# Kernel optimization log

Hardware: AMD Instinct MI355X
Metric: run time of the kernel (lower is better)

Reference implementation:

```python
import jax, jax.numpy as jnp
import numpy as np

V = 100000
E = 1600000
IN_CH = 128
HEADS = 4
OUT_CH = 16
NEG_SLOPE = 0.2


def setup_inputs() -> dict:
    key = jax.random.key(0)
    k1, k2, k3, k4, k5 = jax.random.split(key, 5)
    x = jax.random.normal(k1, (V, IN_CH), dtype=jnp.float32)
    edge_index = jax.random.randint(k2, (2, E), 0, V, dtype=jnp.int32)
    # Xavier-ish scaled params
    W = jax.random.normal(k3, (IN_CH, HEADS * OUT_CH), dtype=jnp.float32) / np.sqrt(IN_CH)
    a_src = jax.random.normal(k4, (HEADS, OUT_CH), dtype=jnp.float32) / np.sqrt(OUT_CH)
    a_dst = jax.random.normal(k5, (HEADS, OUT_CH), dtype=jnp.float32) / np.sqrt(OUT_CH)
    return {"x": x, "edge_index": edge_index, "W": W, "a_src": a_src, "a_dst": a_dst}


def reference(x, edge_index, W, a_src, a_dst):
    v = x.shape[0]
    h, cout = a_src.shape
    z = (x @ W).reshape(v, h, cout)                      # [V,H,C]
    src, dst = edge_index[0], edge_index[1]
    # per-node attention logits, then gather at edges (same math as gather-then-dot)
    e_src = jnp.einsum("vhc,hc->vh", z, a_src)           # [V,H]
    e_dst = jnp.einsum("vhc,hc->vh", z, a_dst)           # [V,H]
    e = jax.nn.leaky_relu(e_src[src] + e_dst[dst], NEG_SLOPE)  # [E,H]
    # scatter softmax over dst per head
    m = jax.ops.segment_max(e, dst, num_segments=v)      # [V,H]
    # nodes with no incoming edges get -inf max; edges never reference them
    exp_e = jnp.exp(e - m[dst])                          # [E,H]
    denom = jax.ops.segment_sum(exp_e, dst, num_segments=v)  # [V,H]
    alpha = exp_e / (denom[dst] + 1e-9)                  # [E,H]
    # scatter aggregation of weighted source features
    agg = jax.ops.segment_sum(z[src] * alpha[:, :, None], dst, num_segments=v)  # [V,H,C]
    out = jax.nn.elu(agg)
    return out.reshape(v, h * cout)
```

## Files before the change

### kernel.cpp

```cpp
#include <hip/hip_runtime.h>
#include <hip/hip_bf16.h>
#include <cstdint>

#define NV 100000
#define NE 1600000
#define KIN 128
#define NH 4
#define NC 16
#define NF 64
#define NBKT 782
#define BCAP 2432
#define EPW 16
#define BINWG 391
#define GEMMWG 1563
#define XSTR 136

typedef __attribute__((ext_vector_type(8))) short bf16x8;
typedef __attribute__((ext_vector_type(4))) float f32x4;

__device__ __forceinline__ short f2bf(float f) {
    unsigned u = __float_as_uint(f);
    return (short)((u + 0x7FFFu + ((u >> 16) & 1u)) >> 16);
}

__device__ __forceinline__ unsigned enc11(float w) {
    unsigned t = (__float_as_uint(w) + 0x10000u) >> 17;
    t = min(max(t, 7168u), 9215u);
    return t - 7168u;
}

__global__ __launch_bounds__(256) void k_prep(
    const float* __restrict__ W, short* __restrict__ wfrag,
    int* __restrict__ gcur)
{
    const int t = threadIdx.x;
    for (int i = t; i < NBKT; i += 256) gcur[i] = 0;
#pragma unroll
    for (int it = 0; it < 4; ++it) {
        const int idx = it * 256 + t;
        const int lane = idx & 63;
        const int ctks = idx >> 6;
        const int ct = ctks >> 2, ks = ctks & 3;
        const int n = lane & 15, quad = lane >> 4;
        short* dst = wfrag + (size_t)idx * 8;
#pragma unroll
        for (int j = 0; j < 8; ++j) {
            const int k = ks * 32 + quad * 8 + j;
            dst[j] = f2bf(W[k * NF + ct * 16 + n]);
        }
    }
}

__global__ __launch_bounds__(256) void k_front(
    const float* __restrict__ x, const short* __restrict__ wfrag,
    const float* __restrict__ a_src, const float* __restrict__ a_dst,
    __hip_bfloat16* __restrict__ z, float* __restrict__ esrc,
    float* __restrict__ edst,
    const int* __restrict__ ei, int* __restrict__ gcur,
    unsigned* __restrict__ barr)
{
    if (blockIdx.x % 5 == 0) {
        __shared__ int hist[NBKT];
        __shared__ int base[NBKT];
        const int t = threadIdx.x;
        const int e0 = (blockIdx.x / 5) * (256 * EPW);

        for (int i = t; i < NBKT; i += 256) hist[i] = 0;
        __syncthreads();

        unsigned pk[EPW];
        short bk[EPW];
#pragma unroll
        for (int i = 0; i < EPW; ++i) {
            const int e = e0 + i * 256 + t;
            if (e < NE) {
                const int s = ei[e];
                const int d = ei[NE + e];
                const int b = d >> 7;
                bk[i] = (short)b;
                pk[i] = ((unsigned)(d & 127) << 17) | (unsigned)s;
                atomicAdd(&hist[b], 1);
            } else {
                bk[i] = -1;
            }
        }
        __syncthreads();
        for (int i = t; i < NBKT; i += 256) {
            const int c = hist[i];
            base[i] = c ? atomicAdd(&gcur[i], c) : 0;
            hist[i] = 0;
        }
        __syncthreads();
#pragma unroll
        for (int i = 0; i < EPW; ++i) {
            if (bk[i] >= 0) {
                const int b = bk[i];
                const int pos = base[b] + atomicAdd(&hist[b], 1);
                barr[(size_t)b * BCAP + pos] = pk[i];
            }
        }
    } else {
        __shared__ short xs[64 * XSTR];
        const int t = threadIdx.x;
        const int bb = blockIdx.x - blockIdx.x / 5 - 1;
        const float4* __restrict__ x4 = (const float4*)x;

#pragma unroll
        for (int i = 0; i < 8; ++i) {
            const int li = i * 256 + t;
            const int idx = bb * 2048 + li;
            float4 v = make_float4(0.f, 0.f, 0.f, 0.f);
            if (idx < NV * (KIN / 4)) v = x4[idx];
            short* p = &xs[(li >> 5) * XSTR + (li & 31) * 4];
            p[0] = f2bf(v.x); p[1] = f2bf(v.y);
            p[2] = f2bf(v.z); p[3] = f2bf(v.w);
        }
        __syncthreads();

        const int wv = t >> 6;
        const int lane = t & 63;
        const int n = lane & 15;
        const int quad = lane >> 4;

        bf16x8 bf[16];
        const bf16x8* __restrict__ wf = (const bf16x8*)wfrag;
#pragma unroll
        for (int i = 0; i < 16; ++i) bf[i] = wf[i * 64 + lane];

        const short* __restrict__ arow = &xs[(wv * 16 + n) * XSTR];
        f32x4 acc[4];
#pragma unroll
        for (int ct = 0; ct < 4; ++ct) acc[ct] = (f32x4){0.f, 0.f, 0.f, 0.f};

#pragma unroll
        for (int ks = 0; ks < 4; ++ks) {
            const bf16x8 af = *(const bf16x8*)(arow + ks * 32 + quad * 8);
#pragma unroll
            for (int ct = 0; ct < 4; ++ct)
                acc[ct] = __builtin_amdgcn_mfma_f32_16x16x32_bf16(
                    af, bf[ct * 4 + ks], acc[ct], 0, 0, 0);
        }

        float as[4], ad[4];
#pragma unroll
        for (int ct = 0; ct < 4; ++ct) {
            as[ct] = a_src[ct * 16 + n];
            ad[ct] = a_dst[ct * 16 + n];
        }
        unsigned short* __restrict__ zz = (unsigned short*)z;
#pragma unroll
        for (int ct = 0; ct < 4; ++ct) {
#pragma unroll
            for (int reg = 0; reg < 4; ++reg) {
                const int r_g = bb * 64 + wv * 16 + quad * 4 + reg;
                const float v = acc[ct][reg];
                float ps = v * as[ct];
                float pd = v * ad[ct];
#pragma unroll
                for (int m = 8; m >= 1; m >>= 1) {
                    ps += __shfl_xor(ps, m, 16);
                    pd += __shfl_xor(pd, m, 16);
                }
                if (r_g < NV) {
                    zz[(size_t)r_g * NF + ct * 16 + n] = (unsigned short)f2bf(v);
                    if (n == 0) {
                        esrc[r_g * NH + ct] = ps;
                        edst[r_g * NH + ct] = pd;
                    }
                }
            }
        }
    }
}

__global__ __launch_bounds__(512) void k_back(
    const int* __restrict__ gcur, const unsigned* __restrict__ barr,
    const float* __restrict__ esrc, const float* __restrict__ edst,
    const __hip_bfloat16* __restrict__ z, float* __restrict__ out)
{
    __shared__ unsigned arr[BCAP];
    __shared__ unsigned long long rec[BCAP];
    __shared__ int hist[128], off[128], cur[128];
    __shared__ float4 led[128];
    const int t = threadIdx.x;
    const int b = blockIdx.x;
    const int f = gcur[b];
    const unsigned* __restrict__ bp = barr + (size_t)b * BCAP;

    for (int i = t; i < f; i += 512) arr[i] = bp[i];
    if (t < 128) {
        hist[t] = 0;
        cur[t] = 0;
        const int d = b * 128 + t;
        led[t] = (d < NV) ? *(const float4*)(edst + (size_t)d * 4)
                          : make_float4(0.f, 0.f, 0.f, 0.f);
    }
    __syncthreads();
    for (int i = t; i < f; i += 512) atomicAdd(&hist[arr[i] >> 17], 1);
    __syncthreads();
    if (t < 128) off[t] = hist[t];
    __syncthreads();
    for (int s = 1; s < 128; s <<= 1) {
        const int v = (t < 128 && t >= s) ? off[t - s] : 0;
        __syncthreads();
        if (t < 128) off[t] += v;
        __syncthreads();
    }
    if (t < 128) off[t] -= hist[t];
    __syncthreads();

    for (int i = t; i < f; i += 512) {
        const unsigned p = arr[i];
        const int dl = p >> 17;
        const unsigned s = p & 0x1FFFFu;
        const int slot = off[dl] + atomicAdd(&cur[dl], 1);
        const float4 e4 = *(const float4*)(esrc + (size_t)s * 4);
        const float4 ed = led[dl];
        float ev;
        ev = e4.x + ed.x; ev = ev > 0.f ? ev : 0.2f * ev;
        const unsigned w0 = enc11(__expf(ev));
        ev = e4.y + ed.y; ev = ev > 0.f ? ev : 0.2f * ev;
        const unsigned w1 = enc11(__expf(ev));
        ev = e4.z + ed.z; ev = ev > 0.f ? ev : 0.2f * ev;
        const unsigned w2 = enc11(__expf(ev));
        ev = e4.w + ed.w; ev = ev > 0.f ? ev : 0.2f * ev;
        const unsigned w3 = enc11(__expf(ev));
        rec[slot] = (unsigned long long)s
            | ((unsigned long long)w0 << 17)
            | ((unsigned long long)w1 << 28)
            | ((unsigned long long)w2 << 39)
            | ((unsigned long long)w3 << 50);
    }
    __syncthreads();

    const int wv = t >> 6;
    const int lane = t & 63;
    const int quad = lane >> 4;
    const int li = lane & 15;
    const int sh = 17 + 11 * (li >> 2);
    const unsigned short* __restrict__ z16 = (const unsigned short*)z;

    for (int k = 0; k < 16; ++k) {
        const int dl = wv + k * 8;
        const int d = b * 128 + dl;
        const int begin = off[dl];
        const int nd = hist[dl];
        float a0 = 0.f, a1 = 0.f, a2 = 0.f, a3 = 0.f, den = 0.f;
        for (int j = 0; j < nd; j += 4) {
            const int je = j + quad;
            unsigned long long r = 0ull;
            if (je < nd) r = rec[begin + je];
            const unsigned s = (unsigned)r & 0x1FFFFu;
            const unsigned wu = ((unsigned)(r >> sh)) & 0x7FFu;
            const float w = __uint_as_float((wu + 7168u) << 17);
            const uint2 zv = *(const uint2*)(z16 + ((size_t)s << 6) + li * 4);
            a0 = fmaf(w, __uint_as_float(zv.x << 16), a0);
            a1 = fmaf(w, __uint_as_float(zv.x & 0xFFFF0000u), a1);
            a2 = fmaf(w, __uint_as_float(zv.y << 16), a2);
            a3 = fmaf(w, __uint_as_float(zv.y & 0xFFFF0000u), a3);
            den += w;
        }
        a0 += __shfl_xor(a0, 16); a0 += __shfl_xor(a0, 32);
        a1 += __shfl_xor(a1, 16); a1 += __shfl_xor(a1, 32);
        a2 += __shfl_xor(a2, 16); a2 += __shfl_xor(a2, 32);
        a3 += __shfl_xor(a3, 16); a3 += __shfl_xor(a3, 32);
        den += __shfl_xor(den, 16); den += __shfl_xor(den, 32);
        if (lane < 16 && d < NV) {
            const float id = 1.f / (den + 1e-9f);
            float v0 = a0 * id, v1 = a1 * id, v2 = a2 * id, v3 = a3 * id;
            v0 = v0 > 0.f ? v0 : __expf(v0) - 1.f;
            v1 = v1 > 0.f ? v1 : __expf(v1) - 1.f;
            v2 = v2 > 0.f ? v2 : __expf(v2) - 1.f;
            v3 = v3 > 0.f ? v3 : __expf(v3) - 1.f;
            *(float4*)(out + (size_t)d * NF + li * 4) =
                make_float4(v0, v1, v2, v3);
        }
    }
}

extern "C" void kernel_launch(void* const* d_in, const int* in_sizes, int n_in,
                              void* d_out, int out_size, void* d_ws, size_t ws_size,
                              hipStream_t stream)
{
    const float* x     = (const float*)d_in[0];
    const int*   ei    = (const int*)d_in[1];
    const float* W     = (const float*)d_in[2];
    const float* a_src = (const float*)d_in[3];
    const float* a_dst = (const float*)d_in[4];
    float* out = (float*)d_out;

    char* p = (char*)d_ws;
    __hip_bfloat16* z = (__hip_bfloat16*)p;  p += (size_t)NV * NF * 2;
    float* esrc = (float*)p;                 p += (size_t)NV * NH * 4;
    float* edst = (float*)p;                 p += (size_t)NV * NH * 4;
    int*   gcur = (int*)p;                   p += (size_t)NBKT * 4;
    p = (char*)(((uintptr_t)p + 255) & ~(uintptr_t)255);
    short* wfrag = (short*)p;                p += (size_t)1024 * 8 * 2;
    p = (char*)(((uintptr_t)p + 255) & ~(uintptr_t)255);
    unsigned* barr = (unsigned*)p;           p += (size_t)NBKT * BCAP * 4;

    k_prep<<<1, 256, 0, stream>>>(W, wfrag, gcur);
    k_front<<<BINWG + GEMMWG, 256, 0, stream>>>(x, wfrag, a_src, a_dst, z,
                                                esrc, edst, ei, gcur, barr);
    k_back<<<NBKT, 512, 0, stream>>>(gcur, barr, esrc, edst, z, out);
}
```

Baseline: 178.2 us.

## Fold attention projections into GEMM, halve bucket size, unroll aggregation loop

```diff
diff --git a/kernel.cpp b/kernel.cpp
--- a/kernel.cpp
+++ b/kernel.cpp
@@ -8,8 +8,8 @@
 #define NH 4
 #define NC 16
 #define NF 64
-#define NBKT 782
-#define BCAP 2432
+#define NBKT 1563
+#define BCAP 1216
 #define EPW 16
 #define BINWG 391
 #define GEMMWG 1563
@@ -30,38 +30,51 @@
 }
 
 __global__ __launch_bounds__(256) void k_prep(
-    const float* __restrict__ W, short* __restrict__ wfrag,
+    const float* __restrict__ W, const float* __restrict__ a_src,
+    const float* __restrict__ a_dst, short* __restrict__ wfrag,
     int* __restrict__ gcur)
 {
-    const int t = threadIdx.x;
-    for (int i = t; i < NBKT; i += 256) gcur[i] = 0;
-#pragma unroll
-    for (int it = 0; it < 4; ++it) {
-        const int idx = it * 256 + t;
-        const int lane = idx & 63;
-        const int ctks = idx >> 6;
+    const int g = blockIdx.x * 256 + threadIdx.x;
+    if (g < NBKT) gcur[g] = 0;
+    if (g < 1280) {
+        const int lane = g & 63;
+        const int ctks = g >> 6;
         const int ct = ctks >> 2, ks = ctks & 3;
         const int n = lane & 15, quad = lane >> 4;
-        short* dst = wfrag + (size_t)idx * 8;
+        short* dst = wfrag + (size_t)g * 8;
 #pragma unroll
         for (int j = 0; j < 8; ++j) {
             const int k = ks * 32 + quad * 8 + j;
-            dst[j] = f2bf(W[k * NF + ct * 16 + n]);
+            float v = 0.f;
+            if (ct < 4) {
+                v = W[k * NF + ct * 16 + n];
+            } else if (n < 8) {
+                const int h = n & 3;
+                const float* __restrict__ a =
+                    (n < 4) ? (a_src + h * 16) : (a_dst + h * 16);
+                for (int c = 0; c < 16; ++c)
+                    v += W[k * NF + h * 16 + c] * a[c];
+            }
+            dst[j] = f2bf(v);
         }
     }
 }
 
 __global__ __launch_bounds__(256) void k_front(
     const float* __restrict__ x, const short* __restrict__ wfrag,
-    const float* __restrict__ a_src, const float* __restrict__ a_dst,
     __hip_bfloat16* __restrict__ z, float* __restrict__ esrc,
     float* __restrict__ edst,
     const int* __restrict__ ei, int* __restrict__ gcur,
     unsigned* __restrict__ barr)
 {
+    __shared__ union SM {
+        struct { int hist[NBKT]; int base[NBKT]; } bin;
+        short xs[64 * XSTR];
+    } sm;
+
     if (blockIdx.x % 5 == 0) {
-        __shared__ int hist[NBKT];
-        __shared__ int base[NBKT];
+        int* hist = sm.bin.hist;
+        int* base = sm.bin.base;
         const int t = threadIdx.x;
         const int e0 = (blockIdx.x / 5) * (256 * EPW);
 
@@ -76,10 +89,10 @@
             if (e < NE) {
                 const int s = ei[e];
                 const int d = ei[NE + e];
-                const int b = d >> 7;
-                bk[i] = (short)b;
-                pk[i] = ((unsigned)(d & 127) << 17) | (unsigned)s;
-                atomicAdd(&hist[b], 1);
+                const int bkt = d >> 6;
+                bk[i] = (short)bkt;
+                pk[i] = ((unsigned)(d & 63) << 17) | (unsigned)s;
+                atomicAdd(&hist[bkt], 1);
             } else {
                 bk[i] = -1;
             }
@@ -94,13 +107,14 @@
 #pragma unroll
         for (int i = 0; i < EPW; ++i) {
             if (bk[i] >= 0) {
-                const int b = bk[i];
-                const int pos = base[b] + atomicAdd(&hist[b], 1);
-                barr[(size_t)b * BCAP + pos] = pk[i];
+                const int bkt = bk[i];
+                const int pos = base[bkt] + atomicAdd(&hist[bkt], 1);
+                if (pos < BCAP)
+                    barr[(size_t)bkt * BCAP + pos] = pk[i];
             }
         }
     } else {
-        __shared__ short xs[64 * XSTR];
+        short* xs = sm.xs;
         const int t = threadIdx.x;
         const int bb = blockIdx.x - blockIdx.x / 5 - 1;
         const float4* __restrict__ x4 = (const float4*)x;
@@ -111,9 +125,11 @@
             const int idx = bb * 2048 + li;
             float4 v = make_float4(0.f, 0.f, 0.f, 0.f);
             if (idx < NV * (KIN / 4)) v = x4[idx];
-            short* p = &xs[(li >> 5) * XSTR + (li & 31) * 4];
-            p[0] = f2bf(v.x); p[1] = f2bf(v.y);
-            p[2] = f2bf(v.z); p[3] = f2bf(v.w);
+            const unsigned lo = (unsigned)(unsigned short)f2bf(v.x)
+                              | ((unsigned)(unsigned short)f2bf(v.y) << 16);
+            const unsigned hi = (unsigned)(unsigned short)f2bf(v.z)
+                              | ((unsigned)(unsigned short)f2bf(v.w) << 16);
+            *(uint2*)&xs[(li >> 5) * XSTR + (li & 31) * 4] = make_uint2(lo, hi);
         }
         __syncthreads();
 
@@ -122,94 +138,97 @@
         const int n = lane & 15;
         const int quad = lane >> 4;
 
-        bf16x8 bf[16];
+        bf16x8 bf[20];
         const bf16x8* __restrict__ wf = (const bf16x8*)wfrag;
 #pragma unroll
-        for (int i = 0; i < 16; ++i) bf[i] = wf[i * 64 + lane];
+        for (int i = 0; i < 20; ++i) bf[i] = wf[i * 64 + lane];
 
         const short* __restrict__ arow = &xs[(wv * 16 + n) * XSTR];
-        f32x4 acc[4];
-#pragma unroll
-        for (int ct = 0; ct < 4; ++ct) acc[ct] = (f32x4){0.f, 0.f, 0.f, 0.f};
+        f32x4 acc[5];
+#pragma unroll
+        for (int ct = 0; ct < 5; ++ct) acc[ct] = (f32x4){0.f, 0.f, 0.f, 0.f};
 
 #pragma unroll
         for (int ks = 0; ks < 4; ++ks) {
             const bf16x8 af = *(const bf16x8*)(arow + ks * 32 + quad * 8);
 #pragma unroll
-            for (int ct = 0; ct < 4; ++ct)
+            for (int ct = 0; ct < 5; ++ct)
                 acc[ct] = __builtin_amdgcn_mfma_f32_16x16x32_bf16(
                     af, bf[ct * 4 + ks], acc[ct], 0, 0, 0);
         }
 
-        float as[4], ad[4];
-#pragma unroll
-        for (int ct = 0; ct < 4; ++ct) {
-            as[ct] = a_src[ct * 16 + n];
-            ad[ct] = a_dst[ct * 16 + n];
-        }
         unsigned short* __restrict__ zz = (unsigned short*)z;
 #pragma unroll
         for (int ct = 0; ct < 4; ++ct) {
 #pragma unroll
             for (int reg = 0; reg < 4; ++reg) {
                 const int r_g = bb * 64 + wv * 16 + quad * 4 + reg;
-                const float v = acc[ct][reg];
-                float ps = v * as[ct];
-                float pd = v * ad[ct];
-#pragma unroll
-                for (int m = 8; m >= 1; m >>= 1) {
-                    ps += __shfl_xor(ps, m, 16);
-                    pd += __shfl_xor(pd, m, 16);
-                }
-                if (r_g < NV) {
-                    zz[(size_t)r_g * NF + ct * 16 + n] = (unsigned short)f2bf(v);
-                    if (n == 0) {
-                        esrc[r_g * NH + ct] = ps;
-                        edst[r_g * NH + ct] = pd;
-                    }
-                }
-            }
-        }
-    }
-}
-
-__global__ __launch_bounds__(512) void k_back(
+                if (r_g < NV)
+                    zz[(size_t)r_g * NF + ct * 16 + n] =
+                        (unsigned short)f2bf(acc[ct][reg]);
+            }
+        }
+#pragma unroll
+        for (int reg = 0; reg < 4; ++reg) {
+            const int r_g = bb * 64 + wv * 16 + quad * 4 + reg;
+            if (r_g < NV && n < 8) {
+                const float v = acc[4][reg];
+                if (n < 4) esrc[r_g * NH + n] = v;
+                else       edst[r_g * NH + (n - 4)] = v;
+            }
+        }
+    }
+}
+
+__global__ __launch_bounds__(256) void k_back(
     const int* __restrict__ gcur, const unsigned* __restrict__ barr,
     const float* __restrict__ esrc, const float* __restrict__ edst,
     const __hip_bfloat16* __restrict__ z, float* __restrict__ out)
 {
-    __shared__ unsigned arr[BCAP];
+    __shared__ __align__(16) unsigned arr[BCAP];
     __shared__ unsigned long long rec[BCAP];
-    __shared__ int hist[128], off[128], cur[128];
-    __shared__ float4 led[128];
+    __shared__ int hist[64], off[64], cur[64];
+    __shared__ float4 led[64];
     const int t = threadIdx.x;
     const int b = blockIdx.x;
-    const int f = gcur[b];
+    int f = gcur[b]; if (f > BCAP) f = BCAP;
     const unsigned* __restrict__ bp = barr + (size_t)b * BCAP;
 
-    for (int i = t; i < f; i += 512) arr[i] = bp[i];
-    if (t < 128) {
+    if (t < 64) {
         hist[t] = 0;
         cur[t] = 0;
-        const int d = b * 128 + t;
+        const int d = b * 64 + t;
         led[t] = (d < NV) ? *(const float4*)(edst + (size_t)d * 4)
                           : make_float4(0.f, 0.f, 0.f, 0.f);
     }
     __syncthreads();
-    for (int i = t; i < f; i += 512) atomicAdd(&hist[arr[i] >> 17], 1);
-    __syncthreads();
-    if (t < 128) off[t] = hist[t];
-    __syncthreads();
-    for (int s = 1; s < 128; s <<= 1) {
-        const int v = (t < 128 && t >= s) ? off[t - s] : 0;
-        __syncthreads();
-        if (t < 128) off[t] += v;
-        __syncthreads();
-    }
-    if (t < 128) off[t] -= hist[t];
-    __syncthreads();
-
-    for (int i = t; i < f; i += 512) {
+    const int f4 = f >> 2;
+    for (int i = t; i < f4; i += 256) {
+        const uint4 v = ((const uint4*)bp)[i];
+        ((uint4*)arr)[i] = v;
+        atomicAdd(&hist[v.x >> 17], 1);
+        atomicAdd(&hist[v.y >> 17], 1);
+        atomicAdd(&hist[v.z >> 17], 1);
+        atomicAdd(&hist[v.w >> 17], 1);
+    }
+    for (int i = (f4 << 2) + t; i < f; i += 256) {
+        const unsigned v = bp[i];
+        arr[i] = v;
+        atomicAdd(&hist[v >> 17], 1);
+    }
+    __syncthreads();
+    if (t < 64) off[t] = hist[t];
+    __syncthreads();
+    for (int s = 1; s < 64; s <<= 1) {
+        const int v = (t < 64 && t >= s) ? off[t - s] : 0;
+        __syncthreads();
+        if (t < 64) off[t] += v;
+        __syncthreads();
+    }
+    if (t < 64) off[t] -= hist[t];
+    __syncthreads();
+
+    for (int i = t; i < f; i += 256) {
         const unsigned p = arr[i];
         const int dl = p >> 17;
         const unsigned s = p & 0x1FFFFu;
@@ -238,27 +257,37 @@
     const int quad = lane >> 4;
     const int li = lane & 15;
     const int sh = 17 + 11 * (li >> 2);
-    const unsigned short* __restrict__ z16 = (const unsigned short*)z;
+    const unsigned short* __restrict__ zb = (const unsigned short*)z + li * 4;
 
     for (int k = 0; k < 16; ++k) {
-        const int dl = wv + k * 8;
-        const int d = b * 128 + dl;
+        const int dl = (k << 2) | wv;
+        const int d = b * 64 + dl;
         const int begin = off[dl];
         const int nd = hist[dl];
         float a0 = 0.f, a1 = 0.f, a2 = 0.f, a3 = 0.f, den = 0.f;
-        for (int j = 0; j < nd; j += 4) {
-            const int je = j + quad;
-            unsigned long long r = 0ull;
-            if (je < nd) r = rec[begin + je];
-            const unsigned s = (unsigned)r & 0x1FFFFu;
-            const unsigned wu = ((unsigned)(r >> sh)) & 0x7FFu;
-            const float w = __uint_as_float((wu + 7168u) << 17);
-            const uint2 zv = *(const uint2*)(z16 + ((size_t)s << 6) + li * 4);
-            a0 = fmaf(w, __uint_as_float(zv.x << 16), a0);
-            a1 = fmaf(w, __uint_as_float(zv.x & 0xFFFF0000u), a1);
-            a2 = fmaf(w, __uint_as_float(zv.y << 16), a2);
-            a3 = fmaf(w, __uint_as_float(zv.y & 0xFFFF0000u), a3);
-            den += w;
+        for (int j = 0; j < nd; j += 8) {
+            const int je0 = j + quad;
+            const int je1 = je0 + 4;
+            const unsigned long long r0 = (je0 < nd) ? rec[begin + je0] : 0ull;
+            const unsigned long long r1 = (je1 < nd) ? rec[begin + je1] : 0ull;
+            const unsigned s0 = (unsigned)r0 & 0x1FFFFu;
+            const unsigned s1 = (unsigned)r1 & 0x1FFFFu;
+            const float w0 = __uint_as_float(
+                ((((unsigned)(r0 >> sh)) & 0x7FFu) + 7168u) << 17);
+            const float w1 = __uint_as_float(
+                ((((unsigned)(r1 >> sh)) & 0x7FFu) + 7168u) << 17);
+            const uint2 zv0 = *(const uint2*)(zb + ((size_t)s0 << 6));
+            const uint2 zv1 = *(const uint2*)(zb + ((size_t)s1 << 6));
+            a0 = fmaf(w0, __uint_as_float(zv0.x << 16), a0);
+            a1 = fmaf(w0, __uint_as_float(zv0.x & 0xFFFF0000u), a1);
+            a2 = fmaf(w0, __uint_as_float(zv0.y << 16), a2);
+            a3 = fmaf(w0, __uint_as_float(zv0.y & 0xFFFF0000u), a3);
+            den += w0;
+            a0 = fmaf(w1, __uint_as_float(zv1.x << 16), a0);
+            a1 = fmaf(w1, __uint_as_float(zv1.x & 0xFFFF0000u), a1);
+            a2 = fmaf(w1, __uint_as_float(zv1.y << 16), a2);
+            a3 = fmaf(w1, __uint_as_float(zv1.y & 0xFFFF0000u), a3);
+            den += w1;
         }
         a0 += __shfl_xor(a0, 16); a0 += __shfl_xor(a0, 32);
         a1 += __shfl_xor(a1, 16); a1 += __shfl_xor(a1, 32);
@@ -295,12 +324,12 @@
     float* edst = (float*)p;                 p += (size_t)NV * NH * 4;
     int*   gcur = (int*)p;                   p += (size_t)NBKT * 4;
     p = (char*)(((uintptr_t)p + 255) & ~(uintptr_t)255);
-    short* wfrag = (short*)p;                p += (size_t)1024 * 8 * 2;
+    short* wfrag = (short*)p;                p += (size_t)1280 * 8 * 2;
     p = (char*)(((uintptr_t)p + 255) & ~(uintptr_t)255);
     unsigned* barr = (unsigned*)p;           p += (size_t)NBKT * BCAP * 4;
 
-    k_prep<<<1, 256, 0, stream>>>(W, wfrag, gcur);
-    k_front<<<BINWG + GEMMWG, 256, 0, stream>>>(x, wfrag, a_src, a_dst, z,
-                                                esrc, edst, ei, gcur, barr);
-    k_back<<<NBKT, 512, 0, stream>>>(gcur, barr, esrc, edst, z, out);
-}
+    k_prep<<<7, 256, 0, stream>>>(W, a_src, a_dst, wfrag, gcur);
+    k_front<<<BINWG + GEMMWG, 256, 0, stream>>>(x, wfrag, z, esrc, edst,
+                                                ei, gcur, barr);
+    k_back<<<NBKT, 256, 0, stream>>>(gcur, barr, esrc, edst, z, out);
+}
```

Measured after the change: 179.2 us. About the same (+0.5%).
